# Kernel optimization log

Measured on AMD Instinct MI355X. Metric: run time of the kernel, lower is better.

Reference implementation:

```python
import jax, jax.numpy as jnp
import numpy as np

H = 768   # config.hidden_size
B = 1024  # batch
S = 256   # attention context length
C1, C2, C3 = 202, 183, 11  # num_class for crit, law, time


def setup_inputs() -> dict:
    key = jax.random.key(0)
    ks = jax.random.split(key, 18)
    sd = 1.0 / np.sqrt(H)
    def u(k, shape):
        return jax.random.uniform(k, shape, jnp.float32, -sd, sd)
    return {
        "x": jax.random.normal(ks[0], (B, H), jnp.float32),
        "attn": jax.random.normal(ks[1], (B, S, H), jnp.float32),
        # 3 LSTMCells (tasks crit, law, time), stacked
        "Wih": u(ks[2], (3, 4 * H, H)),
        "Whh": u(ks[3], (3, 4 * H, H)),
        "bih": u(ks[4], (3, 4 * H)),
        "bhh": u(ks[5], (3, 4 * H)),
        # edge (2->3) hidden/cell state Linear (only edge whose FC is reached)
        "hfc_W": u(ks[6], (H, H)), "hfc_b": u(ks[7], (H,)),
        "cfc_W": u(ks[8], (H, H)), "cfc_b": u(ks[9], (H,)),
        # midfc per task
        "midfc_W": u(ks[10], (3, H, H)), "midfc_b": u(ks[11], (3, H)),
        # outfc per task (distinct class counts)
        "out1_W": u(ks[12], (C1, H)), "out1_b": u(ks[13], (C1,)),
        "out2_W": u(ks[14], (C2, H)), "out2_b": u(ks[15], (C2,)),
        "out3_W": u(ks[16], (C3, H)), "out3_b": u(ks[17], (C3,)),
    }


def _lstm_cell(x, h, c, Wih, Whh, bih, bhh):
    # torch nn.LSTMCell: gate order i, f, g, o
    gates = x @ Wih.T + bih + h @ Whh.T + bhh
    i, f, g, o = jnp.split(gates, 4, axis=-1)
    c_new = jax.nn.sigmoid(f) * c + jax.nn.sigmoid(i) * jnp.tanh(g)
    h_new = jax.nn.sigmoid(o) * jnp.tanh(c_new)
    return h_new, c_new


def _attend(h, attn):
    # Attention: ratio = softmax(bmm(attn, h)); result = bmm(attn^T, ratio)
    w = jax.nn.softmax(jnp.einsum('bsh,bh->bs', attn, h), axis=1)
    return jnp.einsum('bsh,bs->bh', attn, w)


def _head(h, mW, mb, oW, ob):
    # more_fc=True: outfc(relu(midfc(h)))
    return jax.nn.relu(h @ mW.T + mb) @ oW.T + ob


def reference(x, attn, Wih, Whh, bih, bhh, hfc_W, hfc_b, cfc_W, cfc_b,
              midfc_W, midfc_b, out1_W, out1_b, out2_W, out2_b, out3_W, out3_b):
    # graph "[(1 2),(1 3),(2 3)]": edges 1->2, 1->3, 2->3; initial hidden_list all zero.
    z = jnp.zeros_like(x)
    # task 1 (crit): runs on zero state; first-touch sets hidden[2]=hidden[3]=(h1,c1)
    h1, c1 = _lstm_cell(x, z, z, Wih[0], Whh[0], bih[0], bhh[0])
    # task 2 (law): state = (h1, c1)
    h2, c2 = _lstm_cell(x, h1, c1, Wih[1], Whh[1], bih[1], bhh[1])
    # edge 2->3 applies the per-edge Linear and accumulates into hidden[3]
    hp3 = h1 + h2 @ hfc_W.T + hfc_b
    cp3 = c1 + c2 @ cfc_W.T + cfc_b
    # task 3 (time)
    h3, c3 = _lstm_cell(x, hp3, cp3, Wih[2], Whh[2], bih[2], bhh[2])
    # attention over encoder context, per task head
    a1 = _attend(h1, attn)
    a2 = _attend(h2, attn)
    a3 = _attend(h3, attn)
    o1 = _head(a1, midfc_W[0], midfc_b[0], out1_W, out1_b)
    o2 = _head(a2, midfc_W[1], midfc_b[1], out2_W, out2_b)
    o3 = _head(a3, midfc_W[2], midfc_b[2], out3_W, out3_b)
    return (o1, o2, o3)
```

## Files before the change

kernel.cpp:

```cpp
#include <hip/hip_runtime.h>


typedef unsigned short u16;
typedef _Float16       f16x8 __attribute__((ext_vector_type(8)));
typedef float          f32x4 __attribute__((ext_vector_type(4)));

#define SWZ(r) ((((r) + ((r) >> 2))) & 3)
#define VMCNT(N) asm volatile("s_waitcnt vmcnt(" #N ")" ::: "memory")
#define KBAR()  do { __builtin_amdgcn_s_barrier(); __builtin_amdgcn_sched_barrier(0); } while (0)

__device__ __forceinline__ u16 f2h(float f) {
  _Float16 h = (_Float16)f;
  return __builtin_bit_cast(u16, h);
}
__device__ __forceinline__ float sigm(float x) { return 1.f / (1.f + __expf(-x)); }
__device__ __forceinline__ float ftanh(float x) { return 1.f - 2.f / (__expf(2.f * x) + 1.f); }

__device__ __forceinline__ void gld16(const u16* g, u16* l) {
  __builtin_amdgcn_global_load_lds(
      (const __attribute__((address_space(1))) unsigned int*)(g),
      (__attribute__((address_space(3))) unsigned int*)(l),
      16, 0, 0);
}

struct KP64 { const u16 *pA, *pW; };

__device__ __forceinline__ void stage64(const KP64& kp, int kt,
                                        u16* Asb, u16* Bsb, int wv) {
  const int off = kt * 32;
  gld16(kp.pA + off, Asb + wv * 512);
  gld16(kp.pW + off, Bsb + wv * 512);
}

__device__ __forceinline__ void compute64(const u16* Asb, const u16* Bsb,
                                          int wv, int frow, int fsl, f32x4* acc) {
  const int ar = wv * 16 + frow;
  f16x8 ah = *(const f16x8*)(Asb + ar * 32 + ((fsl ^ SWZ(ar)) * 8));
  f16x8 bh[4];
#pragma unroll
  for (int n = 0; n < 4; ++n) {
    const int br = n * 16 + frow;
    bh[n] = *(const f16x8*)(Bsb + br * 32 + ((fsl ^ SWZ(br)) * 8));
  }
#pragma unroll
  for (int n = 0; n < 4; ++n)
    acc[n] = __builtin_amdgcn_mfma_f32_16x16x32_f16(ah, bh[n], acc[n], 0, 0, 0);
}

__device__ __forceinline__ void kloop64(const KP64& kp, int NT, u16* As, u16* Bs,
                                        int wv, int frow, int fsl, f32x4* acc) {
  stage64(kp, 0, As,        Bs,        wv);
  stage64(kp, 1, As + 2048, Bs + 2048, wv);
  stage64(kp, 2, As + 4096, Bs + 4096, wv);
  for (int t = 0; t < NT - 2; ++t) {
    VMCNT(4); KBAR();
    const int cb = t & 3;
    compute64(As + cb * 2048, Bs + cb * 2048, wv, frow, fsl, acc);
    if (t + 3 < NT) {
      const int sb = (t + 3) & 3;
      stage64(kp, t + 3, As + sb * 2048, Bs + sb * 2048, wv);
    }
  }
  VMCNT(2); KBAR();
  compute64(As + ((NT - 2) & 3) * 2048, Bs + ((NT - 2) & 3) * 2048,
            wv, frow, fsl, acc);
  VMCNT(0); KBAR();
  compute64(As + ((NT - 1) & 3) * 2048, Bs + ((NT - 1) & 3) * 2048,
            wv, frow, fsl, acc);
}

struct GJob {
  const u16* A; const u16* W;
  float* outf; u16* outh;
  const float* bias; const float* bias2; const float* addend;
  int N; int ldc; int relu;
};

__device__ __forceinline__ void run_gemm64(const GJob& jb, int bx, int by,
                                           u16* As, u16* Bs, int tid) {
  const int bn0 = bx * 64;
  if (bn0 >= jb.N) return;
  const int bm0 = by * 64;
  const int lane = tid & 63, wv = tid >> 6;
  const int frow = lane & 15, fsl = lane >> 4;

  const int ra = tid >> 2, csa = (tid & 3) ^ SWZ(ra);
  int wr = bn0 + ra; if (wr >= jb.N) wr = jb.N - 1;

  KP64 kp;
  kp.pA = jb.A + (size_t)(bm0 + ra) * 768 + csa * 8;
  kp.pW = jb.W + (size_t)wr * 768 + csa * 8;

  f32x4 acc[4];
#pragma unroll
  for (int n = 0; n < 4; ++n) acc[n] = (f32x4){0.f, 0.f, 0.f, 0.f};

  kloop64(kp, 24, As, Bs, wv, frow, fsl, acc);

  const int rb = (lane >> 4) * 4;
  const int cc = lane & 15;
#pragma unroll
  for (int n = 0; n < 4; ++n) {
    const int col = bn0 + n * 16 + cc;
    if (col >= jb.N) continue;
    float bv = 0.f;
    if (jb.bias)  bv += jb.bias[col];
    if (jb.bias2) bv += jb.bias2[col];
    const int row0 = bm0 + wv * 16 + rb;
#pragma unroll
    for (int r = 0; r < 4; ++r) {
      const int row = row0 + r;
      float v = acc[n][r] + bv;
      if (jb.addend) v += jb.addend[(size_t)row * jb.ldc + col];
      if (jb.relu)   v = fmaxf(v, 0.f);
      if (jb.outf)   jb.outf[(size_t)row * jb.ldc + col] = v;
      if (jb.outh)   jb.outh[(size_t)row * jb.ldc + col] = f2h(v);
    }
  }
}

__device__ __forceinline__ void run_cell64(const u16* A, const u16* W,
                                           const float* bi, const float* bh_,
                                           const float* addend,
                                           const float* cprev,
                                           float* hf, float* cf, u16* hh, u16* ch,
                                           int bx, int by,
                                           u16* As, u16* Bs, int tid) {
  const int bj0 = bx * 16;
  const int bm0 = by * 64;
  const int lane = tid & 63, wv = tid >> 6;
  const int frow = lane & 15, fsl = lane >> 4;

  const int ra = tid >> 2, csa = (tid & 3) ^ SWZ(ra);
  const int wr = (ra >> 4) * 768 + bj0 + (ra & 15);

  KP64 kp;
  kp.pA = A + (size_t)(bm0 + ra) * 768 + csa * 8;
  kp.pW = W + (size_t)wr * 768 + csa * 8;

  f32x4 acc[4];
#pragma unroll
  for (int n = 0; n < 4; ++n) acc[n] = (f32x4){0.f, 0.f, 0.f, 0.f};

  kloop64(kp, 24, As, Bs, wv, frow, fsl, acc);

  const int rb = (lane >> 4) * 4;
  const int cc = lane & 15;
  const int j = bj0 + cc;
  float b_i = 0.f, b_f = 0.f, b_g = 0.f, b_o = 0.f;
  if (bi) {
    b_i = bi[j]        + bh_[j];
    b_f = bi[768 + j]  + bh_[768 + j];
    b_g = bi[1536 + j] + bh_[1536 + j];
    b_o = bi[2304 + j] + bh_[2304 + j];
  }
  const int row0 = bm0 + wv * 16 + rb;
#pragma unroll
  for (int r = 0; r < 4; ++r) {
    const int row = row0 + r;
    float gi = acc[0][r] + b_i;
    float gf = acc[1][r] + b_f;
    float gg = acc[2][r] + b_g;
    float go = acc[3][r] + b_o;
    if (addend) {
      const float* ad = addend + (size_t)row * 6144;
      gi += ad[j]; gf += ad[768 + j]; gg += ad[1536 + j]; go += ad[2304 + j];
    }
    float c = sigm(gi) * ftanh(gg);
    if (cprev) c += sigm(gf) * cprev[row * 768 + j];
    float h = sigm(go) * ftanh(c);
    if (hf) hf[row * 768 + j] = h;
    if (cf) cf[row * 768 + j] = c;
    if (hh) hh[row * 768 + j] = f2h(h);
    if (ch) ch[row * 768 + j] = f2h(c);
  }
}

__device__ __forceinline__ void cvt_seg(const float* s, u16* d, int n4,
                                        int gtid, int nthr) {
  for (int i = gtid; i < n4; i += nthr) {
    float4 v = ((const float4*)s)[i];
    ushort4 h;
    h.x = f2h(v.x); h.y = f2h(v.y); h.z = f2h(v.z); h.w = f2h(v.w);
    ((ushort4*)d)[i] = h;
  }
}

__global__ __launch_bounds__(256)
void cvt0_k(const float* x, u16* xh, const float* Wih, u16* Wihh)
{
  const int g = blockIdx.x * 256 + threadIdx.x, N = 2048 * 256;
  cvt_seg(x,   xh,   196608,  g, N);
  cvt_seg(Wih, Wihh, 1769472, g, N);
}

struct K1P {
  const u16 *xh, *Wihh;
  const float *bih, *bhh;
  float *h1f, *c1f; u16* h1h;
  float* Gpre;
  const float *Whh, *hfcW, *cfcW, *midW, *o1W, *o2W, *o3W;
  u16 *Whhh, *hfch, *cfch, *midh, *o1h, *o2h, *o3h;
};

__global__ __launch_bounds__(256)
void k1_k(K1P p)
{
  __shared__ __align__(16) u16 As[8192];
  __shared__ __align__(16) u16 Bs[8192];
  const int blk = blockIdx.x, tid = threadIdx.x;

  if (blk < 768) {
    run_cell64(p.xh, p.Wihh, p.bih, p.bhh, nullptr, nullptr,
               p.h1f, p.c1f, p.h1h, nullptr, blk % 48, blk / 48, As, Bs, tid);
  } else if (blk < 1536) {
    const int r = blk - 768;
    GJob jb = { p.xh, p.Wihh + (size_t)3072 * 768, p.Gpre, nullptr,
                p.bih + 3072, p.bhh + 3072, nullptr, 3072, 6144, 0 };
    run_gemm64(jb, r % 48, r / 48, As, Bs, tid);
  } else {
    const int g = (blk - 1536) * 256 + tid, N = 384 * 256;
    cvt_seg(p.Whh + 2359296, p.Whhh, 1179648, g, N);
    cvt_seg(p.hfcW, p.hfch, 147456, g, N);
    cvt_seg(p.cfcW, p.cfch, 147456, g, N);
    cvt_seg(p.midW, p.midh, 442368, g, N);
    cvt_seg(p.o1W,  p.o1h,  38784,  g, N);
    cvt_seg(p.o2W,  p.o2h,  35136,  g, N);
    cvt_seg(p.o3W,  p.o3h,  2112,   g, N);
  }
}

struct K2P {
  const u16 *h1h, *Whhh, *xh, *Wihh;
  const float *Gpre_t2, *c1f, *bih, *bhh;
  float *h2f, *Gpre_t3; u16 *h2h, *c2h;
};

__global__ __launch_bounds__(256)
void k2_k(K2P p)
{
  __shared__ __align__(16) u16 As[8192];
  __shared__ __align__(16) u16 Bs[8192];
  const int blk = blockIdx.x, tid = threadIdx.x;

  if (blk < 768) {
    run_cell64(p.h1h, p.Whhh, nullptr, nullptr, p.Gpre_t2, p.c1f,
               p.h2f, nullptr, p.h2h, p.c2h, blk % 48, blk / 48, As, Bs, tid);
  } else {
    const int r = blk - 768;
    GJob jb = { p.xh, p.Wihh + (size_t)6144 * 768, p.Gpre_t3, nullptr,
                p.bih + 6144, p.bhh + 6144, nullptr, 3072, 6144, 0 };
    run_gemm64(jb, r % 48, r / 48, As, Bs, tid);
  }
}

__global__ __launch_bounds__(256)
void cell3_k(const u16* __restrict__ A, const u16* __restrict__ W,
             const float* __restrict__ addend, const float* __restrict__ cprev,
             float* hf)
{
  __shared__ __align__(16) u16 As[8192];
  __shared__ __align__(16) u16 Bs[8192];
  run_cell64(A, W, nullptr, nullptr, addend, cprev, hf, nullptr, nullptr, nullptr,
             blockIdx.x, blockIdx.y, As, Bs, threadIdx.x);
}

struct GArgs { GJob j[3]; };

__global__ __launch_bounds__(256)
void gemm64_k(GArgs P)
{
  __shared__ __align__(16) u16 As[8192];
  __shared__ __align__(16) u16 Bs[8192];
  run_gemm64(P.j[blockIdx.z], blockIdx.x, blockIdx.y, As, Bs, threadIdx.x);
}

__global__ __launch_bounds__(256, 4)
void attn_k(const float* __restrict__ attn,
            const float* __restrict__ h1, const float* __restrict__ h2,
            const float* __restrict__ h3,
            u16* __restrict__ a1, u16* __restrict__ a2, u16* __restrict__ a3)
{
  const int b = blockIdx.x, tid = threadIdx.x;
  const int lane = tid & 63, wv = tid >> 6;
  __shared__ float accW[4][3][768];
  __shared__ float lsumW[4][3];

  const float* ab = attn + (size_t)b * 196608;
  const int cb = lane * 4;

  float4 hh[3][3];
#pragma unroll
  for (int j = 0; j < 3; ++j) {
    hh[0][j] = *(const float4*)(h1 + b * 768 + j * 256 + cb);
    hh[1][j] = *(const float4*)(h2 + b * 768 + j * 256 + cb);
    hh[2][j] = *(const float4*)(h3 + b * 768 + j * 256 + cb);
  }

  float4 acc[3][3];
#pragma unroll
  for (int t3 = 0; t3 < 3; ++t3)
#pragma unroll
    for (int j = 0; j < 3; ++j) acc[t3][j] = (float4){0.f, 0.f, 0.f, 0.f};
  float lsum[3] = {0.f, 0.f, 0.f};

  const int row0 = wv * 64;
  for (int sub = 0; sub < 32; ++sub) {
    const float* rp = ab + (size_t)(row0 + sub * 2) * 768 + cb;
    float4 vv[2][3];
#pragma unroll
    for (int s = 0; s < 2; ++s)
#pragma unroll
      for (int j = 0; j < 3; ++j)
        vv[s][j] = *(const float4*)(rp + s * 768 + j * 256);

    float q[3][2];
#pragma unroll
    for (int t3 = 0; t3 < 3; ++t3)
#pragma unroll
      for (int s = 0; s < 2; ++s) {
        float d = 0.f;
#pragma unroll
        for (int j = 0; j < 3; ++j) {
          d = fmaf(vv[s][j].x, hh[t3][j].x, d);
          d = fmaf(vv[s][j].y, hh[t3][j].y, d);
          d = fmaf(vv[s][j].z, hh[t3][j].z, d);
          d = fmaf(vv[s][j].w, hh[t3][j].w, d);
        }
        q[t3][s] = d;
      }
#pragma unroll
    for (int t3 = 0; t3 < 3; ++t3)
#pragma unroll
      for (int s = 0; s < 2; ++s) {
#pragma unroll
        for (int d = 1; d < 64; d <<= 1)
          q[t3][s] += __shfl_xor(q[t3][s], d);
        q[t3][s] = __expf(q[t3][s]);
      }
#pragma unroll
    for (int t3 = 0; t3 < 3; ++t3)
#pragma unroll
      for (int s = 0; s < 2; ++s) {
        const float pw = q[t3][s];
        lsum[t3] += pw;
#pragma unroll
        for (int j = 0; j < 3; ++j) {
          acc[t3][j].x = fmaf(pw, vv[s][j].x, acc[t3][j].x);
          acc[t3][j].y = fmaf(pw, vv[s][j].y, acc[t3][j].y);
          acc[t3][j].z = fmaf(pw, vv[s][j].z, acc[t3][j].z);
          acc[t3][j].w = fmaf(pw, vv[s][j].w, acc[t3][j].w);
        }
      }
  }

#pragma unroll
  for (int t3 = 0; t3 < 3; ++t3)
#pragma unroll
    for (int j = 0; j < 3; ++j)
      *(float4*)(&accW[wv][t3][j * 256 + cb]) = acc[t3][j];
  if (lane == 0) {
#pragma unroll
    for (int t3 = 0; t3 < 3; ++t3) lsumW[wv][t3] = lsum[t3];
  }
  __syncthreads();

  float ltot[3];
#pragma unroll
  for (int t3 = 0; t3 < 3; ++t3)
    ltot[t3] = lsumW[0][t3] + lsumW[1][t3] + lsumW[2][t3] + lsumW[3][t3];
  u16* outs[3] = { a1, a2, a3 };
#pragma unroll
  for (int cc = 0; cc < 3; ++cc) {
    const int c = tid + cc * 256;
#pragma unroll
    for (int t3 = 0; t3 < 3; ++t3) {
      float s = accW[0][t3][c] + accW[1][t3][c] + accW[2][t3][c] + accW[3][t3][c];
      outs[t3][b * 768 + c] = f2h(s / ltot[t3]);
    }
  }
}

extern "C" void kernel_launch(void* const* d_in, const int* in_sizes, int n_in,
                              void* d_out, int out_size, void* d_ws, size_t ws_size,
                              hipStream_t stream)
{
  const float* x    = (const float*)d_in[0];
  const float* attn = (const float*)d_in[1];
  const float* Wih  = (const float*)d_in[2];
  const float* Whh  = (const float*)d_in[3];
  const float* bih  = (const float*)d_in[4];
  const float* bhh  = (const float*)d_in[5];
  const float* hfcW = (const float*)d_in[6];
  const float* hfcb = (const float*)d_in[7];
  const float* cfcW = (const float*)d_in[8];
  const float* cfcb = (const float*)d_in[9];
  const float* midW = (const float*)d_in[10];
  const float* midb = (const float*)d_in[11];
  const float* o1W  = (const float*)d_in[12];
  const float* o1b  = (const float*)d_in[13];
  const float* o2W  = (const float*)d_in[14];
  const float* o2b  = (const float*)d_in[15];
  const float* o3W  = (const float*)d_in[16];
  const float* o3b  = (const float*)d_in[17];
  float* out = (float*)d_out;
  char*  ws  = (char*)d_ws;

  float* Gpre = (float*)(ws + 0);
  float* h1f  = (float*)(ws + 25165824);
  float* c1f  = (float*)(ws + 28311552);
  float* h2f  = (float*)(ws + 31457280);
  float* cp3f = (float*)(ws + 34603008);
  float* h3f  = (float*)(ws + 37748736);
  u16*   xh   = (u16*)(ws + 40894464);
  u16*   Wihh = (u16*)(ws + 42467328);
  u16*   Whhh = (u16*)(ws + 56623104);
  u16*   hfch = (u16*)(ws + 66060288);
  u16*   cfch = (u16*)(ws + 67239936);
  u16*   midh = (u16*)(ws + 68419584);
  u16*   o1h  = (u16*)(ws + 71958528);
  u16*   o2h  = (u16*)(ws + 72268800);
  u16*   o3h  = (u16*)(ws + 72549888);
  u16*   h1h  = (u16*)(ws + 72566784);
  u16*   h2h  = (u16*)(ws + 74139648);
  u16*   c2h  = (u16*)(ws + 75712512);
  u16*   hp3h = (u16*)(ws + 77285376);
  u16*   a1h  = (u16*)(ws + 78858240);
  u16*   a2h  = (u16*)(ws + 80431104);
  u16*   a3h  = (u16*)(ws + 82003968);
  u16*   m1h  = (u16*)(ws + 83576832);
  u16*   m2h  = (u16*)(ws + 85149696);
  u16*   m3h  = (u16*)(ws + 86722560);

  cvt0_k<<<2048, 256, 0, stream>>>(x, xh, Wih, Wihh);

  K1P p1;
  p1.xh = xh; p1.Wihh = Wihh; p1.bih = bih; p1.bhh = bhh;
  p1.h1f = h1f; p1.c1f = c1f; p1.h1h = h1h; p1.Gpre = Gpre;
  p1.Whh = Whh; p1.hfcW = hfcW; p1.cfcW = cfcW; p1.midW = midW;
  p1.o1W = o1W; p1.o2W = o2W; p1.o3W = o3W;
  p1.Whhh = Whhh; p1.hfch = hfch; p1.cfch = cfch; p1.midh = midh;
  p1.o1h = o1h; p1.o2h = o2h; p1.o3h = o3h;
  k1_k<<<1920, 256, 0, stream>>>(p1);

  K2P p2;
  p2.h1h = h1h; p2.Whhh = Whhh; p2.xh = xh; p2.Wihh = Wihh;
  p2.Gpre_t2 = Gpre; p2.c1f = c1f; p2.bih = bih; p2.bhh = bhh;
  p2.h2f = h2f; p2.Gpre_t3 = Gpre + 3072; p2.h2h = h2h; p2.c2h = c2h;
  k2_k<<<1536, 256, 0, stream>>>(p2);

  GArgs P;
  P = GArgs{};
  P.j[0] = { h2h, hfch, nullptr, hp3h, hfcb, nullptr, h1f, 768, 768, 0 };
  P.j[1] = { c2h, cfch, cp3f, nullptr, cfcb, nullptr, c1f, 768, 768, 0 };
  P.j[2] = P.j[1];
  gemm64_k<<<dim3(12, 16, 2), 256, 0, stream>>>(P);

  cell3_k<<<dim3(48, 16), 256, 0, stream>>>(hp3h, Whhh + 2359296,
                                            Gpre + 3072, cp3f, h3f);

  attn_k<<<1024, 256, 0, stream>>>(attn, h1f, h2f, h3f, a1h, a2h, a3h);

  P = GArgs{};
  P.j[0] = { a1h, midh,           nullptr, m1h, midb,        nullptr, nullptr, 768, 768, 1 };
  P.j[1] = { a2h, midh +  589824, nullptr, m2h, midb +  768, nullptr, nullptr, 768, 768, 1 };
  P.j[2] = { a3h, midh + 1179648, nullptr, m3h, midb + 1536, nullptr, nullptr, 768, 768, 1 };
  gemm64_k<<<dim3(12, 16, 3), 256, 0, stream>>>(P);

  P = GArgs{};
  P.j[0] = { m1h, o1h, out,          nullptr, o1b, nullptr, nullptr, 202, 202, 0 };
  P.j[1] = { m2h, o2h, out + 206848, nullptr, o2b, nullptr, nullptr, 183, 183, 0 };
  P.j[2] = { m3h, o3h, out + 394240, nullptr, o3b, nullptr, nullptr,  11,  11, 0 };
  gemm64_k<<<dim3(4, 16, 3), 256, 0, stream>>>(P);

  (void)in_sizes; (void)n_in; (void)out_size; (void)ws_size;
}
```

Before: 295.6 us.

## Fuse cell3 with attention and mid/out heads using atomic flag dependencies

Merges the third LSTM cell and the attention kernel into one launch. The first 768 blocks compute cell3 tiles and signal per-row-group counters, and every block then waits on the counter for its batch row before attending. The midfc and outfc head GEMMs are likewise merged into one kernel, where the out blocks spin on per-tile flags set by the mid blocks. Attention loads switch to nontemporal loads. This removes two launches and lets later work overlap with earlier tails, but adds spin-waits that can deadlock if producer blocks are not scheduled ahead of the waiting consumers.

```diff
diff --git a/kernel.cpp b/kernel.cpp
--- a/kernel.cpp
+++ b/kernel.cpp
@@ -4,6 +4,7 @@
 typedef unsigned short u16;
 typedef _Float16       f16x8 __attribute__((ext_vector_type(8)));
 typedef float          f32x4 __attribute__((ext_vector_type(4)));
+typedef float          f32x4v __attribute__((ext_vector_type(4)));
 
 #define SWZ(r) ((((r) + ((r) >> 2))) & 3)
 #define VMCNT(N) asm volatile("s_waitcnt vmcnt(" #N ")" ::: "memory")
@@ -21,6 +22,14 @@
       (const __attribute__((address_space(1))) unsigned int*)(g),
       (__attribute__((address_space(3))) unsigned int*)(l),
       16, 0, 0);
+}
+
+__device__ __forceinline__ void flag_release(unsigned* f) {
+  __hip_atomic_fetch_add(f, 1u, __ATOMIC_RELEASE, __HIP_MEMORY_SCOPE_AGENT);
+}
+__device__ __forceinline__ void flag_wait(unsigned* f, unsigned target) {
+  while (__hip_atomic_load(f, __ATOMIC_ACQUIRE, __HIP_MEMORY_SCOPE_AGENT) < target)
+    __builtin_amdgcn_s_sleep(2);
 }
 
 struct KP64 { const u16 *pA, *pW; };
@@ -254,17 +263,6 @@
   }
 }
 
-__global__ __launch_bounds__(256)
-void cell3_k(const u16* __restrict__ A, const u16* __restrict__ W,
-             const float* __restrict__ addend, const float* __restrict__ cprev,
-             float* hf)
-{
-  __shared__ __align__(16) u16 As[8192];
-  __shared__ __align__(16) u16 Bs[8192];
-  run_cell64(A, W, nullptr, nullptr, addend, cprev, hf, nullptr, nullptr, nullptr,
-             blockIdx.x, blockIdx.y, As, Bs, threadIdx.x);
-}
-
 struct GArgs { GJob j[3]; };
 
 __global__ __launch_bounds__(256)
@@ -275,26 +273,48 @@
   run_gemm64(P.j[blockIdx.z], blockIdx.x, blockIdx.y, As, Bs, threadIdx.x);
 }
 
+struct C3AP {
+  const u16 *hp3h, *Whh2h;
+  const float *Gpre_t3, *cp3f;
+  float* h3f;
+  const float *attn, *h1f, *h2f;
+  u16 *a1h, *a2h, *a3h;
+  unsigned* cnt;
+};
+
 __global__ __launch_bounds__(256, 4)
-void attn_k(const float* __restrict__ attn,
-            const float* __restrict__ h1, const float* __restrict__ h2,
-            const float* __restrict__ h3,
-            u16* __restrict__ a1, u16* __restrict__ a2, u16* __restrict__ a3)
-{
-  const int b = blockIdx.x, tid = threadIdx.x;
+void c3attn_k(C3AP p)
+{
+  __shared__ __align__(16) char smem[36912];
+  u16* As = (u16*)smem;
+  u16* Bs = (u16*)(smem + 16384);
+  float* accW  = (float*)smem;
+  float* lsumW = (float*)(smem + 36864);
+
+  const int blk = blockIdx.x, tid = threadIdx.x;
   const int lane = tid & 63, wv = tid >> 6;
-  __shared__ float accW[4][3][768];
-  __shared__ float lsumW[4][3];
-
-  const float* ab = attn + (size_t)b * 196608;
+
+  if (blk < 768) {
+    run_cell64(p.hp3h, p.Whh2h, nullptr, nullptr, p.Gpre_t3, p.cp3f,
+               p.h3f, nullptr, nullptr, nullptr, blk % 48, blk / 48,
+               As, Bs, tid);
+    __syncthreads();
+    if (tid == 0) flag_release(&p.cnt[blk / 48]);
+  }
+
+  const int b = blk;
+  if (tid == 0) flag_wait(&p.cnt[b >> 6], 48u);
+  __syncthreads();
+
+  const float* ab = p.attn + (size_t)b * 196608;
   const int cb = lane * 4;
 
   float4 hh[3][3];
 #pragma unroll
   for (int j = 0; j < 3; ++j) {
-    hh[0][j] = *(const float4*)(h1 + b * 768 + j * 256 + cb);
-    hh[1][j] = *(const float4*)(h2 + b * 768 + j * 256 + cb);
-    hh[2][j] = *(const float4*)(h3 + b * 768 + j * 256 + cb);
+    hh[0][j] = *(const float4*)(p.h1f + b * 768 + j * 256 + cb);
+    hh[1][j] = *(const float4*)(p.h2f + b * 768 + j * 256 + cb);
+    hh[2][j] = *(const float4*)(p.h3f + b * 768 + j * 256 + cb);
   }
 
   float4 acc[3][3];
@@ -307,12 +327,13 @@
   const int row0 = wv * 64;
   for (int sub = 0; sub < 32; ++sub) {
     const float* rp = ab + (size_t)(row0 + sub * 2) * 768 + cb;
-    float4 vv[2][3];
+    f32x4v vv[2][3];
 #pragma unroll
     for (int s = 0; s < 2; ++s)
 #pragma unroll
       for (int j = 0; j < 3; ++j)
-        vv[s][j] = *(const float4*)(rp + s * 768 + j * 256);
+        vv[s][j] = __builtin_nontemporal_load(
+            (const f32x4v*)(rp + s * 768 + j * 256));
 
     float q[3][2];
 #pragma unroll
@@ -354,30 +375,74 @@
       }
   }
 
+  __syncthreads();
 #pragma unroll
   for (int t3 = 0; t3 < 3; ++t3)
 #pragma unroll
     for (int j = 0; j < 3; ++j)
-      *(float4*)(&accW[wv][t3][j * 256 + cb]) = acc[t3][j];
+      *(float4*)(&accW[(wv * 3 + t3) * 768 + j * 256 + cb]) = acc[t3][j];
   if (lane == 0) {
 #pragma unroll
-    for (int t3 = 0; t3 < 3; ++t3) lsumW[wv][t3] = lsum[t3];
+    for (int t3 = 0; t3 < 3; ++t3) lsumW[wv * 3 + t3] = lsum[t3];
   }
   __syncthreads();
 
   float ltot[3];
 #pragma unroll
   for (int t3 = 0; t3 < 3; ++t3)
-    ltot[t3] = lsumW[0][t3] + lsumW[1][t3] + lsumW[2][t3] + lsumW[3][t3];
-  u16* outs[3] = { a1, a2, a3 };
+    ltot[t3] = lsumW[t3] + lsumW[3 + t3] + lsumW[6 + t3] + lsumW[9 + t3];
+  u16* outs[3] = { p.a1h, p.a2h, p.a3h };
 #pragma unroll
   for (int cc = 0; cc < 3; ++cc) {
     const int c = tid + cc * 256;
 #pragma unroll
     for (int t3 = 0; t3 < 3; ++t3) {
-      float s = accW[0][t3][c] + accW[1][t3][c] + accW[2][t3][c] + accW[3][t3][c];
+      float s = accW[t3 * 768 + c] + accW[(3 + t3) * 768 + c] +
+                accW[(6 + t3) * 768 + c] + accW[(9 + t3) * 768 + c];
       outs[t3][b * 768 + c] = f2h(s / ltot[t3]);
     }
+  }
+}
+
+struct HP {
+  const u16 *a1h, *a2h, *a3h, *midh, *o1h, *o2h, *o3h;
+  const float *midb, *o1b, *o2b, *o3b;
+  u16 *m1h, *m2h, *m3h;
+  float* out;
+  unsigned* cnt2;
+};
+
+__global__ __launch_bounds__(256, 4)
+void headso_k(HP p)
+{
+  __shared__ __align__(16) u16 As[8192];
+  __shared__ __align__(16) u16 Bs[8192];
+  const int blk = blockIdx.x, tid = threadIdx.x;
+
+  const u16* aIn[3]  = { p.a1h, p.a2h, p.a3h };
+  u16*       mOut[3] = { p.m1h, p.m2h, p.m3h };
+  const u16* oW[3]   = { p.o1h, p.o2h, p.o3h };
+  const float* oB[3] = { p.o1b, p.o2b, p.o3b };
+  const int   oN[3]  = { 202, 183, 11 };
+  const int   oOff[3] = { 0, 206848, 394240 };
+
+  if (blk < 576) {
+    const int t = blk / 192, rem = blk % 192;
+    const int by = rem / 12, bx = rem % 12;
+    GJob jb = { aIn[t], p.midh + (size_t)t * 589824, nullptr, mOut[t],
+                p.midb + t * 768, nullptr, nullptr, 768, 768, 1 };
+    run_gemm64(jb, bx, by, As, Bs, tid);
+    __syncthreads();
+    if (tid == 0) flag_release(&p.cnt2[t * 16 + by]);
+  } else {
+    const int f = blk - 576;
+    const int t = f / 64, rem = f % 64;
+    const int by = rem / 4, bx = rem % 4;
+    if (tid == 0) flag_wait(&p.cnt2[t * 16 + by], 12u);
+    __syncthreads();
+    GJob jb = { mOut[t], oW[t], p.out + oOff[t], nullptr,
+                oB[t], nullptr, nullptr, oN[t], oN[t], 0 };
+    run_gemm64(jb, bx, by, As, Bs, tid);
   }
 }
 
@@ -431,6 +496,10 @@
   u16*   m1h  = (u16*)(ws + 83576832);
   u16*   m2h  = (u16*)(ws + 85149696);
   u16*   m3h  = (u16*)(ws + 86722560);
+  unsigned* cnt1 = (unsigned*)(ws + 88295424);
+  unsigned* cnt2 = (unsigned*)(ws + 88295488);
+
+  (void)hipMemsetAsync(cnt1, 0, 256, stream);
 
   cvt0_k<<<2048, 256, 0, stream>>>(x, xh, Wih, Wihh);
 
@@ -456,22 +525,21 @@
   P.j[2] = P.j[1];
   gemm64_k<<<dim3(12, 16, 2), 256, 0, stream>>>(P);
 
-  cell3_k<<<dim3(48, 16), 256, 0, stream>>>(hp3h, Whhh + 2359296,
-                                            Gpre + 3072, cp3f, h3f);
-
-  attn_k<<<1024, 256, 0, stream>>>(attn, h1f, h2f, h3f, a1h, a2h, a3h);
-
-  P = GArgs{};
-  P.j[0] = { a1h, midh,           nullptr, m1h, midb,        nullptr, nullptr, 768, 768, 1 };
-  P.j[1] = { a2h, midh +  589824, nullptr, m2h, midb +  768, nullptr, nullptr, 768, 768, 1 };
-  P.j[2] = { a3h, midh + 1179648, nullptr, m3h, midb + 1536, nullptr, nullptr, 768, 768, 1 };
-  gemm64_k<<<dim3(12, 16, 3), 256, 0, stream>>>(P);
-
-  P = GArgs{};
-  P.j[0] = { m1h, o1h, out,          nullptr, o1b, nullptr, nullptr, 202, 202, 0 };
-  P.j[1] = { m2h, o2h, out + 206848, nullptr, o2b, nullptr, nullptr, 183, 183, 0 };
-  P.j[2] = { m3h, o3h, out + 394240, nullptr, o3b, nullptr, nullptr,  11,  11, 0 };
-  gemm64_k<<<dim3(4, 16, 3), 256, 0, stream>>>(P);
+  C3AP p4;
+  p4.hp3h = hp3h; p4.Whh2h = Whhh + 2359296;
+  p4.Gpre_t3 = Gpre + 3072; p4.cp3f = cp3f; p4.h3f = h3f;
+  p4.attn = attn; p4.h1f = h1f; p4.h2f = h2f;
+  p4.a1h = a1h; p4.a2h = a2h; p4.a3h = a3h;
+  p4.cnt = cnt1;
+  c3attn_k<<<1024, 256, 0, stream>>>(p4);
+
+  HP p5;
+  p5.a1h = a1h; p5.a2h = a2h; p5.a3h = a3h; p5.midh = midh;
+  p5.o1h = o1h; p5.o2h = o2h; p5.o3h = o3h;
+  p5.midb = midb; p5.o1b = o1b; p5.o2b = o2b; p5.o3b = o3b;
+  p5.m1h = m1h; p5.m2h = m2h; p5.m3h = m3h;
+  p5.out = out; p5.cnt2 = cnt2;
+  headso_k<<<768, 256, 0, stream>>>(p5);
 
   (void)in_sizes; (void)n_in; (void)out_size; (void)ws_size;
 }
```

Result: slower. 457.0 us (+54.6%).
